# Performance work log

Measured on AMD Instinct MI355X. Metric: run time of the kernel, lower is better.

## Reference

```python
import jax, jax.numpy as jnp
import numpy as np

N = 100_000      # nodes
F_IN = 256       # num_features
HID = 128        # args.hidden
C = 32           # num_classes
E = 1_600_000    # edges
EPS = 0.1        # AntiSymmetricConv epsilon
GAMMA = 0.1      # AntiSymmetricConv gamma


def setup_inputs() -> dict:
    key = jax.random.key(0)
    ks = jax.random.split(key, 10)
    def rn(k, shape, scale=0.05):
        return jax.random.normal(k, shape, dtype=jnp.float32) * scale
    x = jax.random.normal(ks[0], (N, F_IN), dtype=jnp.float32)
    edge_index = jax.random.randint(ks[1], (2, E), 0, N, dtype=jnp.int32)
    return {
        "x": x,
        "lin1_w": rn(ks[2], (HID, F_IN)), "lin1_b": jnp.zeros((HID,), jnp.float32),
        "lin2_w": rn(ks[3], (C, HID)),   "lin2_b": jnp.zeros((C,), jnp.float32),
        "W1": rn(ks[4], (HID, HID)), "phi1_w": rn(ks[5], (HID, HID)), "b1": jnp.zeros((HID,), jnp.float32),
        "W2": rn(ks[6], (C, C)),     "phi2_w": rn(ks[7], (C, C)),     "b2": jnp.zeros((C,), jnp.float32),
        "edge_index": edge_index,
    }


def gcn_norm(edge_index, n):
    # GCNConv default: add self-loops, symmetric D^-1/2 (A+I) D^-1/2 normalization
    loops = jnp.arange(n, dtype=edge_index.dtype)
    row = jnp.concatenate([edge_index[0], loops])  # source
    col = jnp.concatenate([edge_index[1], loops])  # target (aggregation)
    deg = jax.ops.segment_sum(jnp.ones(row.shape[0], jnp.float32), col, num_segments=n)
    dinv = jnp.where(deg > 0, jax.lax.rsqrt(deg), 0.0)
    return row, col, dinv[row] * dinv[col]


def gcn_conv(x, phi_w, row, col, norm):
    xw = x @ phi_w.T                                  # [N, d]
    msgs = norm[:, None] * xw[row]                    # [E+N, d] gather
    return jax.ops.segment_sum(msgs, col, num_segments=x.shape[0])  # scatter-add


def anti_symmetric_conv(x, row, col, norm, W, phi_w, b):
    d = W.shape[0]
    aw = W - W.T - GAMMA * jnp.eye(d, dtype=W.dtype)  # antisymmetric weight
    h = gcn_conv(x, phi_w, row, col, norm)            # phi(x, edge_index)
    h = jnp.tanh(x @ aw.T + h + b)
    return x + EPS * h                                # one Euler step (num_iters=1)


def reference(x, lin1_w, lin1_b, lin2_w, lin2_b, W1, phi1_w, b1, W2, phi2_w, b2, edge_index):
    row, col, norm = gcn_norm(edge_index, x.shape[0])
    h = jax.nn.relu(x @ lin1_w.T + lin1_b)            # dropout is identity in eval
    h = anti_symmetric_conv(h, row, col, norm, W1, phi1_w, b1)
    h = h @ lin2_w.T + lin2_b
    h = anti_symmetric_conv(h, row, col, norm, W2, phi2_w, b2)
    return jax.nn.log_softmax(h, axis=1)
```

## Files before the change

kernel.cpp:

```cpp
#include <hip/hip_runtime.h>
#include <hip/hip_bf16.h>
#include <math.h>

#define N_NODES 100000
#define F_IN    256
#define HID     128
#define NCLS    32
#define NEDGES  1600000
#define EPS_C   0.1f
#define GAMMA_C 0.1f

#define NBK   782
#define CHUNK 4096
#define NCH   391
#define BMAX  4096

typedef __attribute__((ext_vector_type(8))) short short8;
typedef __attribute__((ext_vector_type(4))) float floatx4;

__device__ __forceinline__ float bf2f(unsigned short u) {
    union { unsigned int u; float f; } c;
    c.u = ((unsigned int)u) << 16;
    return c.f;
}
__device__ __forceinline__ unsigned short f2bf(float f) {
    union { float f; unsigned int u; } c; c.f = f;
    unsigned int u = c.u;
    u += 0x7FFFu + ((u >> 16) & 1u);
    return (unsigned short)(u >> 16);
}

__device__ __forceinline__ float ldf(const void* p, size_t i, int md) {
    return md ? ((const float*)p)[i] : bf2f(((const unsigned short*)p)[i]);
}
__device__ __forceinline__ short8 ld8(const void* p, size_t i, int md) {
    if (md) {
        const float* q = (const float*)p + i;
        short8 r;
#pragma unroll
        for (int j = 0; j < 8; ++j) r[j] = (short)f2bf(q[j]);
        return r;
    }
    return *(const short8*)((const unsigned short*)p + i);
}

__global__ void k_detect(const unsigned short* __restrict__ x, int* __restrict__ mode) {
    __shared__ int cnt;
    if (threadIdx.x == 0) cnt = 0;
    __syncthreads();
    float v = fabsf(bf2f(x[2 * threadIdx.x]));
    if (v > 1e4f || !isfinite(v)) atomicAdd(&cnt, 1);
    __syncthreads();
    if (threadIdx.x == 0) *mode = (cnt >= 8) ? 1 : 0;
}

__global__ __launch_bounds__(256) void k_hist2(const int* __restrict__ ecol,
                                               int* __restrict__ hist, int e) {
    __shared__ int lh[NBK];
    for (int i = threadIdx.x; i < NBK; i += 256) lh[i] = 0;
    __syncthreads();
    int base = blockIdx.x * CHUNK;
    int lim = base + CHUNK; if (lim > e) lim = e;
    for (int i = base + threadIdx.x; i < lim; i += 256)
        atomicAdd(&lh[ecol[i] >> 7], 1);
    __syncthreads();
    for (int i = threadIdx.x; i < NBK; i += 256) hist[blockIdx.x * NBK + i] = lh[i];
}

__global__ __launch_bounds__(256) void k_tot(const int* __restrict__ hist, int* __restrict__ tot) {
    __shared__ int s[256];
    int b = blockIdx.x;
    int v = 0;
    for (int blk = threadIdx.x; blk < NCH; blk += 256) v += hist[blk * NBK + b];
    s[threadIdx.x] = v;
    __syncthreads();
#pragma unroll
    for (int off = 128; off > 0; off >>= 1) {
        if (threadIdx.x < off) s[threadIdx.x] += s[threadIdx.x + off];
        __syncthreads();
    }
    if (threadIdx.x == 0) tot[b] = s[0];
}

__global__ void k_bscan(const int* __restrict__ tot, int* __restrict__ bbase) {
    __shared__ int s[1024];
    int v = (threadIdx.x < NBK) ? tot[threadIdx.x] : 0;
    s[threadIdx.x] = v;
    __syncthreads();
#pragma unroll
    for (int off = 1; off < 1024; off <<= 1) {
        int t = (threadIdx.x >= off) ? s[threadIdx.x - off] : 0;
        __syncthreads();
        s[threadIdx.x] += t;
        __syncthreads();
    }
    if (threadIdx.x < NBK) bbase[threadIdx.x] = s[threadIdx.x] - v;
}

__global__ __launch_bounds__(512) void k_colscan(const int* __restrict__ hist,
                                                 const int* __restrict__ bbase,
                                                 int* __restrict__ off) {
    __shared__ int s[512];
    int b = blockIdx.x, t = threadIdx.x;
    int v = (t < NCH) ? hist[t * NBK + b] : 0;
    s[t] = v;
    __syncthreads();
#pragma unroll
    for (int o = 1; o < 512; o <<= 1) {
        int u = (t >= o) ? s[t - o] : 0;
        __syncthreads();
        s[t] += u;
        __syncthreads();
    }
    if (t < NCH) off[t * NBK + b] = s[t] - v + bbase[b];
}

__global__ __launch_bounds__(256) void k_pass3(
    const int* __restrict__ erow, const int* __restrict__ ecol,
    const int* __restrict__ off, unsigned int* __restrict__ pairs, int e)
{
    __shared__ int lh[NBK];
    __shared__ int lex[NBK + 1];
    __shared__ int cur[NBK];
    __shared__ int wsum[256];
    __shared__ unsigned int sp[CHUNK];
    int base = blockIdx.x * CHUNK;
    int lim = base + CHUNK; if (lim > e) lim = e;
    int cnt = lim - base;

    for (int i = threadIdx.x; i < NBK; i += 256) lh[i] = 0;
    __syncthreads();
    for (int i = base + threadIdx.x; i < lim; i += 256)
        atomicAdd(&lh[ecol[i] >> 7], 1);
    __syncthreads();

    int t4 = threadIdx.x * 4;
    int a0 = (t4 + 0 < NBK) ? lh[t4 + 0] : 0;
    int a1 = (t4 + 1 < NBK) ? lh[t4 + 1] : 0;
    int a2 = (t4 + 2 < NBK) ? lh[t4 + 2] : 0;
    int a3 = (t4 + 3 < NBK) ? lh[t4 + 3] : 0;
    int mysum = a0 + a1 + a2 + a3;
    wsum[threadIdx.x] = mysum;
    __syncthreads();
#pragma unroll
    for (int o = 1; o < 256; o <<= 1) {
        int u = (threadIdx.x >= o) ? wsum[threadIdx.x - o] : 0;
        __syncthreads();
        wsum[threadIdx.x] += u;
        __syncthreads();
    }
    int run = wsum[threadIdx.x] - mysum;
    if (t4 + 0 < NBK) { lex[t4 + 0] = run;            cur[t4 + 0] = run; }
    if (t4 + 1 < NBK) { lex[t4 + 1] = run + a0;       cur[t4 + 1] = run + a0; }
    if (t4 + 2 < NBK) { lex[t4 + 2] = run + a0 + a1;  cur[t4 + 2] = run + a0 + a1; }
    if (t4 + 3 < NBK) { lex[t4 + 3] = run + a0 + a1 + a2; cur[t4 + 3] = run + a0 + a1 + a2; }
    if (threadIdx.x == 0) lex[NBK] = cnt;
    __syncthreads();

    for (int i = base + threadIdx.x; i < lim; i += 256) {
        int dst = ecol[i], src = erow[i];
        int b = dst >> 7;
        int p = atomicAdd(&cur[b], 1);
        sp[p] = ((unsigned int)src << 7) | (unsigned int)(dst & 127);
    }
    __syncthreads();

    for (int i = threadIdx.x; i < cnt; i += 256) {
        int loB = 0, hiB = NBK;
        while (hiB - loB > 1) {
            int mid = (loB + hiB) >> 1;
            if (lex[mid] <= i) loB = mid; else hiB = mid;
        }
        pairs[off[blockIdx.x * NBK + loB] + (i - lex[loB])] = sp[i];
    }
}

__global__ __launch_bounds__(256) void k_build(
    const int* __restrict__ tot, const int* __restrict__ bbase,
    const unsigned int* __restrict__ pairs,
    int* __restrict__ srt, int* __restrict__ row_start, int* __restrict__ cend,
    float* __restrict__ dinv, int n)
{
    __shared__ int lh[128];
    __shared__ int lo[128];
    __shared__ unsigned int se[BMAX];
    int b = blockIdx.x;
    int nb = tot[b]; if (nb > BMAX) nb = BMAX;
    int base = bbase[b];
    if (threadIdx.x < 128) lh[threadIdx.x] = 0;
    __syncthreads();
    for (int e = threadIdx.x; e < nb; e += 256) {
        unsigned int pk = pairs[(size_t)base + e];
        se[e] = pk;
        atomicAdd(&lh[pk & 127u], 1);
    }
    __syncthreads();
    if (threadIdx.x < 128) lo[threadIdx.x] = lh[threadIdx.x];
    __syncthreads();
#pragma unroll
    for (int off = 1; off < 128; off <<= 1) {
        int t = (threadIdx.x < 128 && threadIdx.x >= off) ? lo[threadIdx.x - off] : 0;
        __syncthreads();
        if (threadIdx.x < 128) lo[threadIdx.x] += t;
        __syncthreads();
    }
    int node = b * 128 + threadIdx.x;
    if (threadIdx.x < 128 && node < n) {
        int inc = lo[threadIdx.x], cnt = lh[threadIdx.x];
        row_start[node] = base + inc - cnt;
        cend[node]      = base + inc;
        dinv[node]      = rsqrtf((float)cnt + 1.0f);
    }
    __syncthreads();
    if (threadIdx.x < 128) lh[threadIdx.x] = lo[threadIdx.x] - lh[threadIdx.x];
    __syncthreads();
    for (int e = threadIdx.x; e < nb; e += 256) {
        unsigned int pk = se[e];
        int pos = atomicAdd(&lh[pk & 127u], 1);
        srt[base + pos] = (int)(pk >> 7);
    }
}

__global__ void k_aw(const void* __restrict__ W, unsigned short* __restrict__ aw,
                     const int* __restrict__ dmode, int d) {
    int idx = blockIdx.x * blockDim.x + threadIdx.x;
    if (idx >= d * d) return;
    int md = dmode[0];
    int n = idx / d, k = idx - n * d;
    float v = ldf(W, n * d + k, md) - ldf(W, k * d + n, md) - ((n == k) ? GAMMA_C : 0.0f);
    aw[idx] = f2bf(v);
}

template<int K, int NC, int EPI, bool APOLY, bool BPOLY, int RT, int KTILE>
__global__ __launch_bounds__(256) void k_gemm3(
    const void* A, const void* B, const void* bias,
    unsigned short* Cout,
    const unsigned short* agg, const unsigned short* xw, const float* dinv,
    const int* dmode, void* opout, int M)
{
    constexpr int KP = KTILE + 8;
    constexpr int NT = NC / 16;
    constexpr int KS = KTILE / 32;
    constexpr int RPB = 64 * RT;
    __shared__ __align__(16) unsigned short sB[NC * KP];
    const int md = dmode[0];

    const int lane = threadIdx.x & 63;
    const int wave = threadIdx.x >> 6;
    const int l15  = lane & 15;
    const int quad = lane >> 4;
    const int row0 = blockIdx.x * RPB + wave * (16 * RT);

    int am[RT];
#pragma unroll
    for (int rt = 0; rt < RT; ++rt) {
        int r = row0 + rt * 16 + l15;
        am[rt] = r < M ? r : M - 1;
    }

    floatx4 acc[RT][NT];
#pragma unroll
    for (int rt = 0; rt < RT; ++rt)
#pragma unroll
        for (int t = 0; t < NT; ++t) acc[rt][t] = (floatx4){0.f, 0.f, 0.f, 0.f};

    for (int kt = 0; kt < K; kt += KTILE) {
        short8 a[KS][RT];
#pragma unroll
        for (int s = 0; s < KS; ++s)
#pragma unroll
            for (int rt = 0; rt < RT; ++rt)
                a[s][rt] = APOLY ? ld8(A, (size_t)am[rt] * K + kt + s * 32 + quad * 8, md)
                                 : *(const short8*)((const unsigned short*)A +
                                       (size_t)am[rt] * K + kt + s * 32 + quad * 8);

        if (kt > 0) __syncthreads();
        for (int base = threadIdx.x * 8; base < NC * KTILE; base += 2048) {
            int r = base / KTILE, c = base - r * KTILE;
            if (BPOLY && md) {
                const float* q = (const float*)B + (size_t)r * K + kt + c;
#pragma unroll
                for (int j = 0; j < 8; ++j) sB[r * KP + c + j] = f2bf(q[j]);
            } else {
                *(short8*)(sB + r * KP + c) =
                    *(const short8*)((const unsigned short*)B + (size_t)r * K + kt + c);
            }
        }
        __syncthreads();

#pragma unroll
        for (int s = 0; s < KS; ++s) {
            short8 b[NT];
#pragma unroll
            for (int t = 0; t < NT; ++t)
                b[t] = *(const short8*)(sB + (t * 16 + l15) * KP + s * 32 + quad * 8);
#pragma unroll
            for (int rt = 0; rt < RT; ++rt)
#pragma unroll
                for (int t = 0; t < NT; ++t)
                    acc[rt][t] = __builtin_amdgcn_mfma_f32_16x16x32_bf16(a[s][rt], b[t], acc[rt][t], 0, 0, 0);
        }
    }

    const unsigned short* Ares = (const unsigned short*)A;
#pragma unroll
    for (int rt = 0; rt < RT; ++rt) {
#pragma unroll
        for (int reg = 0; reg < 4; ++reg) {
            int rr = row0 + rt * 16 + quad * 4 + reg;
            if (EPI == 4) {
                int rrc = rr < M ? rr : M - 1;
                float dv = dinv[rrc];
                float val[NT];
#pragma unroll
                for (int t = 0; t < NT; ++t) {
                    int col = t * 16 + l15;
                    float z = acc[rt][t][reg]
                            + bf2f(agg[(size_t)rrc * NC + col])
                            + dv * bf2f(xw[(size_t)rrc * NC + col])
                            + ldf(bias, col, md);
                    val[t] = bf2f(Ares[(size_t)rrc * K + col]) + EPS_C * tanhf(z);
                }
                float m = val[0];
#pragma unroll
                for (int t = 1; t < NT; ++t) m = fmaxf(m, val[t]);
#pragma unroll
                for (int msk = 1; msk < 16; msk <<= 1) m = fmaxf(m, __shfl_xor(m, msk));
                float s = 0.f;
#pragma unroll
                for (int t = 0; t < NT; ++t) s += expf(val[t] - m);
#pragma unroll
                for (int msk = 1; msk < 16; msk <<= 1) s += __shfl_xor(s, msk);
                float ls = m + logf(s);
                if (rr < M) {
#pragma unroll
                    for (int t = 0; t < NT; ++t) {
                        int col = t * 16 + l15;
                        float r = val[t] - ls;
                        if (md) ((float*)opout)[(size_t)rr * NC + col] = r;
                        else    ((unsigned short*)opout)[(size_t)rr * NC + col] = f2bf(r);
                    }
                }
            } else {
                if (rr >= M) continue;
#pragma unroll
                for (int t = 0; t < NT; ++t) {
                    int col = t * 16 + l15;
                    float v = acc[rt][t][reg];
                    if (EPI == 0) { v += ldf(bias, col, md); v = v > 0.f ? v : 0.f; }
                    else if (EPI == 2) { v += ldf(bias, col, md); }
                    else if (EPI == 5) { v *= dinv[rr]; }
                    else if (EPI == 3) {
                        float dv = dinv[rr];
                        float z = v + bf2f(agg[(size_t)rr * NC + col])
                                + dv * bf2f(xw[(size_t)rr * NC + col])
                                + ldf(bias, col, md);
                        v = bf2f(Ares[(size_t)rr * K + col]) + EPS_C * tanhf(z);
                    }
                    Cout[(size_t)rr * NC + col] = f2bf(v);
                }
            }
        }
    }
}

__global__ __launch_bounds__(256) void k_lin2phi2(
    const unsigned short* __restrict__ A, const void* __restrict__ B1,
    const void* __restrict__ bias, const void* __restrict__ B2,
    unsigned short* __restrict__ h3, unsigned short* __restrict__ xws2,
    const float* __restrict__ dinv, const int* __restrict__ dmode, int M)
{
    constexpr int K1 = 128, KP1 = 136, KP2 = 40;
    __shared__ __align__(16) unsigned short sB1[32 * KP1];
    __shared__ __align__(16) unsigned short sB2[32 * KP2];
    __shared__ __align__(16) unsigned short sT[128 * KP2];
    const int md = dmode[0];

    const int lane = threadIdx.x & 63;
    const int wave = threadIdx.x >> 6;
    const int l15  = lane & 15;
    const int quad = lane >> 4;
    const int row0 = blockIdx.x * 128 + wave * 32;

    int am[2];
#pragma unroll
    for (int rt = 0; rt < 2; ++rt) {
        int r = row0 + rt * 16 + l15;
        am[rt] = r < M ? r : M - 1;
    }

    short8 a1[4][2];
#pragma unroll
    for (int s = 0; s < 4; ++s)
#pragma unroll
        for (int rt = 0; rt < 2; ++rt)
            a1[s][rt] = *(const short8*)(A + (size_t)am[rt] * K1 + s * 32 + quad * 8);

    for (int base = threadIdx.x * 8; base < 32 * K1; base += 2048) {
        int r = base / K1, c = base - r * K1;
        if (md) {
            const float* q = (const float*)B1 + base;
#pragma unroll
            for (int j = 0; j < 8; ++j) sB1[r * KP1 + c + j] = f2bf(q[j]);
        } else {
            *(short8*)(sB1 + r * KP1 + c) = *(const short8*)((const unsigned short*)B1 + base);
        }
    }
    for (int base = threadIdx.x * 8; base < 32 * 32; base += 2048) {
        int r = base / 32, c = base - r * 32;
        if (md) {
            const float* q = (const float*)B2 + base;
#pragma unroll
            for (int j = 0; j < 8; ++j) sB2[r * KP2 + c + j] = f2bf(q[j]);
        } else {
            *(short8*)(sB2 + r * KP2 + c) = *(const short8*)((const unsigned short*)B2 + base);
        }
    }
    __syncthreads();

    floatx4 acc[2][2];
#pragma unroll
    for (int rt = 0; rt < 2; ++rt) { acc[rt][0] = (floatx4){0,0,0,0}; acc[rt][1] = (floatx4){0,0,0,0}; }

#pragma unroll
    for (int s = 0; s < 4; ++s) {
#pragma unroll
        for (int rt = 0; rt < 2; ++rt) {
#pragma unroll
            for (int t = 0; t < 2; ++t) {
                short8 b = *(const short8*)(sB1 + (t * 16 + l15) * KP1 + s * 32 + quad * 8);
                acc[rt][t] = __builtin_amdgcn_mfma_f32_16x16x32_bf16(a1[s][rt], b, acc[rt][t], 0, 0, 0);
            }
        }
    }
#pragma unroll
    for (int rt = 0; rt < 2; ++rt)
#pragma unroll
        for (int reg = 0; reg < 4; ++reg) {
            int rr = row0 + rt * 16 + quad * 4 + reg;
            int lr = wave * 32 + rt * 16 + quad * 4 + reg;
#pragma unroll
            for (int t = 0; t < 2; ++t) {
                int col = t * 16 + l15;
                unsigned short hv = f2bf(acc[rt][t][reg] + ldf(bias, col, md));
                sT[lr * KP2 + col] = hv;
                if (rr < M) h3[(size_t)rr * 32 + col] = hv;
            }
        }
    __syncthreads();

    floatx4 a2[2][2];
#pragma unroll
    for (int rt = 0; rt < 2; ++rt) {
        short8 a = *(const short8*)(sT + (wave * 32 + rt * 16 + l15) * KP2 + quad * 8);
#pragma unroll
        for (int t = 0; t < 2; ++t) {
            short8 b = *(const short8*)(sB2 + (t * 16 + l15) * KP2 + quad * 8);
            a2[rt][t] = __builtin_amdgcn_mfma_f32_16x16x32_bf16(a, b, (floatx4){0,0,0,0}, 0, 0, 0);
        }
    }
#pragma unroll
    for (int rt = 0; rt < 2; ++rt)
#pragma unroll
        for (int reg = 0; reg < 4; ++reg) {
            int rr = row0 + rt * 16 + quad * 4 + reg;
            if (rr >= M) continue;
            float dv = dinv[rr];
#pragma unroll
            for (int t = 0; t < 2; ++t)
                xws2[(size_t)rr * 32 + t * 16 + l15] = f2bf(dv * a2[rt][t][reg]);
        }
}

__global__ __launch_bounds__(256) void k_gather128(
    const int* __restrict__ srt, const int* __restrict__ rs,
    const int* __restrict__ cend,
    const unsigned short* __restrict__ xws, const float* __restrict__ dinv,
    unsigned short* __restrict__ agg, int n)
{
    int node = blockIdx.x * 8 + (threadIdx.x >> 5);
    int l = threadIdx.x & 31;
    if (node >= n) return;
    int j = rs[node], end = cend[node];
    float a0 = 0.f, a1 = 0.f, a2 = 0.f, a3 = 0.f;
    while (j < end) {
        int idx[8];
#pragma unroll
        for (int k = 0; k < 8; ++k) {
            int jj = j + k;
            idx[k] = srt[jj < end ? jj : end - 1];
        }
        uint2 p[8];
#pragma unroll
        for (int k = 0; k < 8; ++k)
            p[k] = *(const uint2*)(xws + (size_t)idx[k] * 128 + l * 4);
#pragma unroll
        for (int k = 0; k < 8; ++k) {
            if (j + k < end) {
                a0 += bf2f((unsigned short)(p[k].x & 0xFFFFu));
                a1 += bf2f((unsigned short)(p[k].x >> 16));
                a2 += bf2f((unsigned short)(p[k].y & 0xFFFFu));
                a3 += bf2f((unsigned short)(p[k].y >> 16));
            }
        }
        j += 8;
    }
    float dn = dinv[node];
    uint2 out;
    out.x = (unsigned int)f2bf(dn * a0) | ((unsigned int)f2bf(dn * a1) << 16);
    out.y = (unsigned int)f2bf(dn * a2) | ((unsigned int)f2bf(dn * a3) << 16);
    *(uint2*)(agg + (size_t)node * 128 + l * 4) = out;
}

__global__ __launch_bounds__(256) void k_gather32(
    const int* __restrict__ srt, const int* __restrict__ rs,
    const int* __restrict__ cend,
    const unsigned short* __restrict__ xws, const float* __restrict__ dinv,
    unsigned short* __restrict__ agg, int n)
{
    int node = blockIdx.x * 16 + (threadIdx.x >> 4);
    int l = threadIdx.x & 15;
    if (node >= n) return;
    int j = rs[node], end = cend[node];
    float a0 = 0.f, a1 = 0.f;
    while (j < end) {
        int idx[8];
#pragma unroll
        for (int k = 0; k < 8; ++k) {
            int jj = j + k;
            idx[k] = srt[jj < end ? jj : end - 1];
        }
        unsigned int p[8];
#pragma unroll
        for (int k = 0; k < 8; ++k)
            p[k] = *(const unsigned int*)(xws + (size_t)idx[k] * 32 + l * 2);
#pragma unroll
        for (int k = 0; k < 8; ++k) {
            if (j + k < end) {
                a0 += bf2f((unsigned short)(p[k] & 0xFFFFu));
                a1 += bf2f((unsigned short)(p[k] >> 16));
            }
        }
        j += 8;
    }
    float dn = dinv[node];
    unsigned int out = (unsigned int)f2bf(dn * a0) | ((unsigned int)f2bf(dn * a1) << 16);
    *(unsigned int*)(agg + (size_t)node * 32 + l * 2) = out;
}

extern "C" void kernel_launch(void* const* d_in, const int* in_sizes, int n_in,
                              void* d_out, int out_size, void* d_ws, size_t ws_size,
                              hipStream_t stream)
{
    const void* x      = d_in[0];
    const void* lin1_w = d_in[1];
    const void* lin1_b = d_in[2];
    const void* lin2_w = d_in[3];
    const void* lin2_b = d_in[4];
    const void* W1     = d_in[5];
    const void* phi1w  = d_in[6];
    const void* b1     = d_in[7];
    const void* W2     = d_in[8];
    const void* phi2w  = d_in[9];
    const void* b2     = d_in[10];
    const int* eidx    = (const int*)d_in[11];
    const int* erow = eidx;
    const int* ecol = eidx + NEDGES;

    char* ws = (char*)d_ws;
    float* dinv          = (float*)ws;
    int*   dmode         = (int*)(ws + 400000);
    unsigned short* aw1  = (unsigned short*)(ws + 401408);
    unsigned short* aw2  = (unsigned short*)(ws + 435200);
    int* tot             = (int*)(ws + 440320);
    int* bbase           = (int*)(ws + 443648);
    int* row_start       = (int*)(ws + 446976);
    int* cend            = (int*)(ws + 846976);
    int* srt             = (int*)(ws + 1246976);
    int* hist            = (int*)(ws + 7646976);
    int* offb            = (int*)(ws + 8870912);
    unsigned short* h1   = (unsigned short*)(ws + 10485760);
    unsigned short* xws1 = h1 + (size_t)N_NODES * HID;
    unsigned short* agg1 = xws1 + (size_t)N_NODES * HID;
    unsigned short* h2   = xws1;
    unsigned short* h3   = h1;
    unsigned short* xws2 = agg1;
    unsigned short* agg2 = agg1 + (size_t)N_NODES * NCLS;
    unsigned int* pairs  = (unsigned int*)agg1;

    const int GB = 256;
    const int NB64 = (N_NODES + 63) / 64;
    k_detect<<<1, 256, 0, stream>>>((const unsigned short*)x, dmode);

    k_hist2<<<NCH, 256, 0, stream>>>(ecol, hist, NEDGES);
    k_tot<<<NBK, 256, 0, stream>>>(hist, tot);
    k_bscan<<<1, 1024, 0, stream>>>(tot, bbase);
    k_colscan<<<NBK, 512, 0, stream>>>(hist, bbase, offb);
    k_pass3<<<NCH, 256, 0, stream>>>(erow, ecol, offb, pairs, NEDGES);
    k_build<<<NBK, 256, 0, stream>>>(tot, bbase, pairs, srt, row_start, cend, dinv, N_NODES);

    k_aw<<<(HID * HID + GB - 1) / GB, GB, 0, stream>>>(W1, aw1, dmode, HID);
    k_aw<<<(NCLS * NCLS + GB - 1) / GB, GB, 0, stream>>>(W2, aw2, dmode, NCLS);

    k_gemm3<256, 128, 0, true, true, 1, 64><<<NB64, 256, 0, stream>>>(
        x, lin1_w, lin1_b, h1, nullptr, nullptr, nullptr, dmode, nullptr, N_NODES);
    k_gemm3<128, 128, 5, false, true, 1, 64><<<NB64, 256, 0, stream>>>(
        h1, phi1w, nullptr, xws1, nullptr, nullptr, dinv, dmode, nullptr, N_NODES);
    k_gather128<<<(N_NODES + 7) / 8, 256, 0, stream>>>(
        srt, row_start, cend, xws1, dinv, agg1, N_NODES);
    k_gemm3<128, 128, 3, false, false, 1, 64><<<NB64, 256, 0, stream>>>(
        h1, aw1, b1, h2, agg1, xws1, dinv, dmode, nullptr, N_NODES);
    k_lin2phi2<<<(N_NODES + 127) / 128, 256, 0, stream>>>(
        h2, lin2_w, lin2_b, phi2w, h3, xws2, dinv, dmode, N_NODES);
    k_gather32<<<(N_NODES + 15) / 16, 256, 0, stream>>>(
        srt, row_start, cend, xws2, dinv, agg2, N_NODES);
    k_gemm3<32, 32, 4, false, false, 1, 32><<<NB64, 256, 0, stream>>>(
        h3, aw2, b2, nullptr, agg2, xws2, dinv, dmode, d_out, N_NODES);
}
```

Baseline: 436.8 us.

## Replace k-tiled GEMM with full-K single-stage GEMM using 512-thread blocks and column split

The k_gemm3 kernel, which loops over K tiles, is replaced by k_gemm5. The new kernel loads the whole B matrix (all of K) into shared memory once, uses 512-thread blocks covering 128 rows, and can split output columns across blocks (NSPLIT). The lin1 GEMM (K=256) is split into two 64-column halves so its shared B tile stays small. This removes the per-tile barriers and B reloads, at the cost of more LDS per block and duplicated A loads in the split case, which may limit occupancy.

Result: no change. 432.4 us (-1.0%).

```diff
diff --git a/kernel.cpp b/kernel.cpp
--- a/kernel.cpp
+++ b/kernel.cpp
@@ -231,134 +231,119 @@
     aw[idx] = f2bf(v);
 }
 
-template<int K, int NC, int EPI, bool APOLY, bool BPOLY, int RT, int KTILE>
-__global__ __launch_bounds__(256) void k_gemm3(
+template<int K, int NCB, int NCF, int EPI, bool APOLY, bool BPOLY, int NSPLIT>
+__global__ __launch_bounds__(512) void k_gemm5(
     const void* A, const void* B, const void* bias,
     unsigned short* Cout,
     const unsigned short* agg, const unsigned short* xw, const float* dinv,
     const int* dmode, void* opout, int M)
 {
-    constexpr int KP = KTILE + 8;
-    constexpr int NT = NC / 16;
-    constexpr int KS = KTILE / 32;
-    constexpr int RPB = 64 * RT;
-    __shared__ __align__(16) unsigned short sB[NC * KP];
+    constexpr int KP = K + 8;
+    constexpr int NT = NCB / 16;
+    constexpr int KS = K / 32;
+    __shared__ __align__(16) unsigned short sB[NCB * KP];
     const int md = dmode[0];
+
+    const int rowblk = (NSPLIT > 1) ? ((int)blockIdx.x / NSPLIT) : (int)blockIdx.x;
+    const int col0   = (NSPLIT > 1) ? ((int)blockIdx.x % NSPLIT) * NCB : 0;
 
     const int lane = threadIdx.x & 63;
     const int wave = threadIdx.x >> 6;
     const int l15  = lane & 15;
     const int quad = lane >> 4;
-    const int row0 = blockIdx.x * RPB + wave * (16 * RT);
-
-    int am[RT];
-#pragma unroll
-    for (int rt = 0; rt < RT; ++rt) {
-        int r = row0 + rt * 16 + l15;
-        am[rt] = r < M ? r : M - 1;
-    }
-
-    floatx4 acc[RT][NT];
-#pragma unroll
-    for (int rt = 0; rt < RT; ++rt)
-#pragma unroll
-        for (int t = 0; t < NT; ++t) acc[rt][t] = (floatx4){0.f, 0.f, 0.f, 0.f};
-
-    for (int kt = 0; kt < K; kt += KTILE) {
-        short8 a[KS][RT];
-#pragma unroll
-        for (int s = 0; s < KS; ++s)
-#pragma unroll
-            for (int rt = 0; rt < RT; ++rt)
-                a[s][rt] = APOLY ? ld8(A, (size_t)am[rt] * K + kt + s * 32 + quad * 8, md)
-                                 : *(const short8*)((const unsigned short*)A +
-                                       (size_t)am[rt] * K + kt + s * 32 + quad * 8);
-
-        if (kt > 0) __syncthreads();
-        for (int base = threadIdx.x * 8; base < NC * KTILE; base += 2048) {
-            int r = base / KTILE, c = base - r * KTILE;
-            if (BPOLY && md) {
-                const float* q = (const float*)B + (size_t)r * K + kt + c;
-#pragma unroll
-                for (int j = 0; j < 8; ++j) sB[r * KP + c + j] = f2bf(q[j]);
-            } else {
-                *(short8*)(sB + r * KP + c) =
-                    *(const short8*)((const unsigned short*)B + (size_t)r * K + kt + c);
+    const int row0 = rowblk * 128 + wave * 16;
+
+    int ar = row0 + l15;
+    int am = ar < M ? ar : M - 1;
+
+    short8 a[KS];
+#pragma unroll
+    for (int s = 0; s < KS; ++s)
+        a[s] = APOLY ? ld8(A, (size_t)am * K + s * 32 + quad * 8, md)
+                     : *(const short8*)((const unsigned short*)A +
+                           (size_t)am * K + s * 32 + quad * 8);
+
+    for (int base = threadIdx.x * 8; base < NCB * K; base += 4096) {
+        int r = base / K, c = base - r * K;
+        if (BPOLY && md) {
+            const float* q = (const float*)B + (size_t)(col0 + r) * K + c;
+#pragma unroll
+            for (int j = 0; j < 8; ++j) sB[r * KP + c + j] = f2bf(q[j]);
+        } else {
+            *(short8*)(sB + r * KP + c) =
+                *(const short8*)((const unsigned short*)B + (size_t)(col0 + r) * K + c);
+        }
+    }
+    __syncthreads();
+
+    floatx4 acc[NT];
+#pragma unroll
+    for (int t = 0; t < NT; ++t) acc[t] = (floatx4){0.f, 0.f, 0.f, 0.f};
+
+#pragma unroll
+    for (int s = 0; s < KS; ++s) {
+        short8 b[NT];
+#pragma unroll
+        for (int t = 0; t < NT; ++t)
+            b[t] = *(const short8*)(sB + (t * 16 + l15) * KP + s * 32 + quad * 8);
+#pragma unroll
+        for (int t = 0; t < NT; ++t)
+            acc[t] = __builtin_amdgcn_mfma_f32_16x16x32_bf16(a[s], b[t], acc[t], 0, 0, 0);
+    }
+
+    const unsigned short* Ares = (const unsigned short*)A;
+#pragma unroll
+    for (int reg = 0; reg < 4; ++reg) {
+        int rr = row0 + quad * 4 + reg;
+        if (EPI == 4) {
+            int rrc = rr < M ? rr : M - 1;
+            float dv = dinv[rrc];
+            float val[NT];
+#pragma unroll
+            for (int t = 0; t < NT; ++t) {
+                int col = t * 16 + l15;
+                float z = acc[t][reg]
+                        + bf2f(agg[(size_t)rrc * NCF + col])
+                        + dv * bf2f(xw[(size_t)rrc * NCF + col])
+                        + ldf(bias, col, md);
+                val[t] = bf2f(Ares[(size_t)rrc * K + col]) + EPS_C * tanhf(z);
             }
-        }
-        __syncthreads();
-
-#pragma unroll
-        for (int s = 0; s < KS; ++s) {
-            short8 b[NT];
-#pragma unroll
-            for (int t = 0; t < NT; ++t)
-                b[t] = *(const short8*)(sB + (t * 16 + l15) * KP + s * 32 + quad * 8);
-#pragma unroll
-            for (int rt = 0; rt < RT; ++rt)
-#pragma unroll
-                for (int t = 0; t < NT; ++t)
-                    acc[rt][t] = __builtin_amdgcn_mfma_f32_16x16x32_bf16(a[s][rt], b[t], acc[rt][t], 0, 0, 0);
-        }
-    }
-
-    const unsigned short* Ares = (const unsigned short*)A;
-#pragma unroll
-    for (int rt = 0; rt < RT; ++rt) {
-#pragma unroll
-        for (int reg = 0; reg < 4; ++reg) {
-            int rr = row0 + rt * 16 + quad * 4 + reg;
-            if (EPI == 4) {
-                int rrc = rr < M ? rr : M - 1;
-                float dv = dinv[rrc];
-                float val[NT];
+            float m = val[0];
+#pragma unroll
+            for (int t = 1; t < NT; ++t) m = fmaxf(m, val[t]);
+#pragma unroll
+            for (int msk = 1; msk < 16; msk <<= 1) m = fmaxf(m, __shfl_xor(m, msk));
+            float s = 0.f;
+#pragma unroll
+            for (int t = 0; t < NT; ++t) s += expf(val[t] - m);
+#pragma unroll
+            for (int msk = 1; msk < 16; msk <<= 1) s += __shfl_xor(s, msk);
+            float ls = m + logf(s);
+            if (rr < M) {
 #pragma unroll
                 for (int t = 0; t < NT; ++t) {
                     int col = t * 16 + l15;
-                    float z = acc[rt][t][reg]
-                            + bf2f(agg[(size_t)rrc * NC + col])
-                            + dv * bf2f(xw[(size_t)rrc * NC + col])
-                            + ldf(bias, col, md);
-                    val[t] = bf2f(Ares[(size_t)rrc * K + col]) + EPS_C * tanhf(z);
+                    float r = val[t] - ls;
+                    if (md) ((float*)opout)[(size_t)rr * NCF + col] = r;
+                    else    ((unsigned short*)opout)[(size_t)rr * NCF + col] = f2bf(r);
                 }
-                float m = val[0];
-#pragma unroll
-                for (int t = 1; t < NT; ++t) m = fmaxf(m, val[t]);
-#pragma unroll
-                for (int msk = 1; msk < 16; msk <<= 1) m = fmaxf(m, __shfl_xor(m, msk));
-                float s = 0.f;
-#pragma unroll
-                for (int t = 0; t < NT; ++t) s += expf(val[t] - m);
-#pragma unroll
-                for (int msk = 1; msk < 16; msk <<= 1) s += __shfl_xor(s, msk);
-                float ls = m + logf(s);
-                if (rr < M) {
-#pragma unroll
-                    for (int t = 0; t < NT; ++t) {
-                        int col = t * 16 + l15;
-                        float r = val[t] - ls;
-                        if (md) ((float*)opout)[(size_t)rr * NC + col] = r;
-                        else    ((unsigned short*)opout)[(size_t)rr * NC + col] = f2bf(r);
-                    }
+            }
+        } else {
+            if (rr >= M) continue;
+#pragma unroll
+            for (int t = 0; t < NT; ++t) {
+                int gcol = col0 + t * 16 + l15;
+                float v = acc[t][reg];
+                if (EPI == 0) { v += ldf(bias, gcol, md); v = v > 0.f ? v : 0.f; }
+                else if (EPI == 5) { v *= dinv[rr]; }
+                else if (EPI == 3) {
+                    float dv = dinv[rr];
+                    float z = v + bf2f(agg[(size_t)rr * NCF + gcol])
+                            + dv * bf2f(xw[(size_t)rr * NCF + gcol])
+                            + ldf(bias, gcol, md);
+                    v = bf2f(Ares[(size_t)rr * K + gcol]) + EPS_C * tanhf(z);
                 }
-            } else {
-                if (rr >= M) continue;
-#pragma unroll
-                for (int t = 0; t < NT; ++t) {
-                    int col = t * 16 + l15;
-                    float v = acc[rt][t][reg];
-                    if (EPI == 0) { v += ldf(bias, col, md); v = v > 0.f ? v : 0.f; }
-                    else if (EPI == 2) { v += ldf(bias, col, md); }
-                    else if (EPI == 5) { v *= dinv[rr]; }
-                    else if (EPI == 3) {
-                        float dv = dinv[rr];
-                        float z = v + bf2f(agg[(size_t)rr * NC + col])
-                                + dv * bf2f(xw[(size_t)rr * NC + col])
-                                + ldf(bias, col, md);
-                        v = bf2f(Ares[(size_t)rr * K + col]) + EPS_C * tanhf(z);
-                    }
-                    Cout[(size_t)rr * NC + col] = f2bf(v);
-                }
+                Cout[(size_t)rr * NCF + gcol] = f2bf(v);
             }
         }
     }
@@ -589,7 +574,7 @@
     unsigned int* pairs  = (unsigned int*)agg1;
 
     const int GB = 256;
-    const int NB64 = (N_NODES + 63) / 64;
+    const int NB5 = (N_NODES + 127) / 128;
     k_detect<<<1, 256, 0, stream>>>((const unsigned short*)x, dmode);
 
     k_hist2<<<NCH, 256, 0, stream>>>(ecol, hist, NEDGES);
@@ -602,18 +587,18 @@
     k_aw<<<(HID * HID + GB - 1) / GB, GB, 0, stream>>>(W1, aw1, dmode, HID);
     k_aw<<<(NCLS * NCLS + GB - 1) / GB, GB, 0, stream>>>(W2, aw2, dmode, NCLS);
 
-    k_gemm3<256, 128, 0, true, true, 1, 64><<<NB64, 256, 0, stream>>>(
+    k_gemm5<256, 64, 128, 0, true, true, 2><<<NB5 * 2, 512, 0, stream>>>(
         x, lin1_w, lin1_b, h1, nullptr, nullptr, nullptr, dmode, nullptr, N_NODES);
-    k_gemm3<128, 128, 5, false, true, 1, 64><<<NB64, 256, 0, stream>>>(
+    k_gemm5<128, 128, 128, 5, false, true, 1><<<NB5, 512, 0, stream>>>(
         h1, phi1w, nullptr, xws1, nullptr, nullptr, dinv, dmode, nullptr, N_NODES);
     k_gather128<<<(N_NODES + 7) / 8, 256, 0, stream>>>(
         srt, row_start, cend, xws1, dinv, agg1, N_NODES);
-    k_gemm3<128, 128, 3, false, false, 1, 64><<<NB64, 256, 0, stream>>>(
+    k_gemm5<128, 128, 128, 3, false, false, 1><<<NB5, 512, 0, stream>>>(
         h1, aw1, b1, h2, agg1, xws1, dinv, dmode, nullptr, N_NODES);
     k_lin2phi2<<<(N_NODES + 127) / 128, 256, 0, stream>>>(
         h2, lin2_w, lin2_b, phi2w, h3, xws2, dinv, dmode, N_NODES);
     k_gather32<<<(N_NODES + 15) / 16, 256, 0, stream>>>(
         srt, row_start, cend, xws2, dinv, agg2, N_NODES);
-    k_gemm3<32, 32, 4, false, false, 1, 32><<<NB64, 256, 0, stream>>>(
+    k_gemm5<32, 32, 32, 4, false, false, 1><<<NB5, 512, 0, stream>>>(
         h3, aw2, b2, nullptr, agg2, xws2, dinv, dmode, d_out, N_NODES);
 }
```
